# Performance work log

Measured on AMD Instinct MI355X. Metric: run time of the kernel, lower is better.

## Reference

```python
import jax, jax.numpy as jnp
import numpy as np


def lrelu(x):
    return jnp.where(x > 0, x, 0.1 * x)


def setup_inputs() -> dict:
    key = jax.random.key(0)
    ks = jax.random.split(key, 16)
    L, B, E = 160, 16, 512
    C, H, DM, DO = 256, 512, 128, 512  # conv channels, enc_hid, d_mlp, dec_hid

    def rn(k, shape, scale=0.05):
        return jax.random.normal(k, shape, dtype=jnp.float32) * scale

    return {
        "x": rn(ks[0], (L, B, E), 1.0),
        "h": rn(ks[1], (B, H), 1.0),
        "conv_w": rn(ks[2], (C, E, 3)),
        "conv_b": rn(ks[3], (C,)),
        "bn_g": jnp.ones((C,), jnp.float32),
        "bn_b": jnp.zeros((C,), jnp.float32),
        "W1": rn(ks[4], (DM, 2 * (C + 2) + H)),
        "b1": rn(ks[5], (DM,)),
        "W2": rn(ks[6], (DM, DM)), "b2": rn(ks[7], (DM,)),
        "W3": rn(ks[8], (DM, DM)), "b3": rn(ks[9], (DM,)),
        "W4": rn(ks[10], (DM, DM)), "b4": rn(ks[11], (DM,)),
        "W5": rn(ks[12], (DM, DM)), "b5": rn(ks[13], (DM,)),
        "W6": rn(ks[14], (DO, DM)), "b6": rn(ks[15], (DO,)),
    }


def reference(x, h, conv_w, conv_b, bn_g, bn_b,
              W1, b1, W2, b2, W3, b3, W4, b4, W5, b5, W6, b6):
    L, B, E = x.shape
    # --- ConvLayer: Conv1d(k=3, pad=1) -> LeakyReLU(0.1) -> BatchNorm1d (training stats)
    xc = jnp.transpose(x, (1, 2, 0))  # (B, E, L)
    y = jax.lax.conv_general_dilated(xc, conv_w, (1,), [(1, 1)],
                                     dimension_numbers=("NCH", "OIH", "NCH"))
    y = lrelu(y + conv_b[None, :, None])
    mu = y.mean(axis=(0, 2), keepdims=True)
    var = y.var(axis=(0, 2), keepdims=True)  # biased variance (torch training BN)
    y = (y - mu) * jax.lax.rsqrt(var + 1e-5)
    y = y * bn_g[None, :, None] + bn_b[None, :, None]
    y = jnp.transpose(y, (0, 2, 1))  # (B, L, C)

    # --- coordinate features: [(i/sqrt(L)-2)/2, (i % sqrt(L) - 2)/2]
    sL = np.sqrt(L)
    i = jnp.arange(L, dtype=jnp.float32)
    coords = jnp.stack([(i / sL - 2.0) / 2.0, (jnp.mod(i, sL) - 2.0) / 2.0], axis=-1)  # (L, 2)
    xf = jnp.concatenate([y, jnp.broadcast_to(coords[None], (B, L, 2))], axis=-1)  # (B, L, C+2)
    Cp = xf.shape[-1]

    # --- g_mlp first Linear decomposed over [x_i | x_j | h] feature blocks:
    # x_i[b,a,c] = xf[b,c] (varies with dim2); x_j[b,a,c] = cat(xf[b,a], h[b]) (varies with dim1)
    W1i = W1[:, :Cp]            # acts on x_i
    W1jx = W1[:, Cp:2 * Cp]     # acts on x part of x_j
    W1jh = W1[:, 2 * Cp:]       # acts on h part of x_j
    u = jnp.einsum('blc,dc->bld', xf, W1i)                     # (B, L, DM), index = dim2
    v = jnp.einsum('blc,dc->bld', xf, W1jx) + (h @ W1jh.T)[:, None, :]  # (B, L, DM), index = dim1
    z = lrelu(v[:, :, None, :] + u[:, None, :, :] + b1)        # (B, L, L, DM)
    z = lrelu(z @ W2.T + b2)
    z = lrelu(z @ W3.T + b3)
    z = lrelu(z @ W4.T + b4)
    s = z.sum(axis=(1, 2))  # sum over all L*L pairs -> (B, DM)

    # --- f_mlp
    s = lrelu(s @ W5.T + b5)
    return lrelu(s @ W6.T + b6)  # (B, dec_hid)
```

## Files before the change

### kernel.cpp

```cpp
#include <hip/hip_runtime.h>
#include <cstdint>

typedef unsigned short u16;
typedef uint32_t u32;

typedef __bf16 bf16x8 __attribute__((ext_vector_type(8)));
typedef float  f32x2  __attribute__((ext_vector_type(2)));
typedef float  f32x4  __attribute__((ext_vector_type(4)));
typedef float  f32x16 __attribute__((ext_vector_type(16)));
typedef u16    u16x4  __attribute__((ext_vector_type(4)));
typedef u16    u16x8  __attribute__((ext_vector_type(8)));

__device__ __forceinline__ u16 f2bf(float f) {
    u32 x = __float_as_uint(f);
    return (u16)((x + 0x7FFFu + ((x >> 16) & 1u)) >> 16);
}
__device__ __forceinline__ float lrelu(float x) { return fmaxf(x, 0.1f * x); }

__device__ __forceinline__ u32 pack_rn(float lo, float hi) {
    u32 a = __float_as_uint(lo) + 0x8000u;
    u32 b = __float_as_uint(hi) + 0x8000u;
    return __builtin_amdgcn_perm(b, a, 0x07060302u);
}

__global__ __launch_bounds__(256) void k_prep(
    const float* __restrict__ x, const float* __restrict__ conv_w,
    const float* __restrict__ W2, const float* __restrict__ W3, const float* __restrict__ W4,
    const float* __restrict__ b2, const float* __restrict__ b3, const float* __restrict__ b4,
    const float* __restrict__ h, const float* __restrict__ W1,
    u16* __restrict__ xb, u16* __restrict__ wcb_f, u16* __restrict__ wfrag,
    float* __restrict__ W1T4, float* __restrict__ hW)
{
    int blk = blockIdx.x, tid = threadIdx.x;
    if (blk < 1280) {
        int o = (blk * 256 + tid) * 4;
        int e = o & 511;
        int bl = o >> 9;
        int b = bl / 160, l = bl % 160;
        f32x4 v = *(const f32x4*)(x + ((size_t)(l * 16 + b)) * 512 + e);
        u16x4 ov;
        ov[0] = f2bf(v[0]); ov[1] = f2bf(v[1]); ov[2] = f2bf(v[2]); ov[3] = f2bf(v[3]);
        *(u16x4*)&xb[o] = ov;
    } else if (blk < 1472) {
        int g = (blk - 1280) * 256 + tid;
        int lane = g & 63;
        int ks = (g >> 6) % 48;
        int cb = g / 3072;
        int c = cb * 16 + (lane & 15);
        int quad = lane >> 4;
        int k0 = ks * 32 + quad * 8;
        int tap = k0 >> 9, e0 = k0 & 511;
        u16x8 ov;
        #pragma unroll
        for (int j = 0; j < 8; j++)
            ov[j] = f2bf(conv_w[((size_t)c * 512 + e0 + j) * 3 + tap]);
        *(u16x8*)&wcb_f[(size_t)g * 8] = ov;
    } else if (blk < 1526) {
        int o = ((blk - 1472) * 256 + tid) * 4;
        int layer = o / 18432, rem = o % 18432;
        int ks9 = rem >> 11;
        int rem2 = rem & 2047;
        int hh = rem2 >> 10;
        int rem3 = rem2 & 1023;
        int n = rem3 >> 3, j0 = rem3 & 7;
        const float* W = (layer == 0) ? W2 : (layer == 1) ? W3 : W4;
        const float* bi = (layer == 0) ? b2 : (layer == 1) ? b3 : b4;
        u16x4 ov;
        if (ks9 < 8) {
            f32x4 v = *(const f32x4*)(W + (size_t)n * 128 + 16 * ks9 + 8 * hh + j0);
            ov[0] = f2bf(v[0]); ov[1] = f2bf(v[1]); ov[2] = f2bf(v[2]); ov[3] = f2bf(v[3]);
        } else {
            ov[0] = (hh == 0 && j0 == 0) ? f2bf(bi[n]) : (u16)0;
            ov[1] = 0; ov[2] = 0; ov[3] = 0;
        }
        *(u16x4*)&wfrag[o] = ov;
    } else if (blk < 1591) {
        int cq = blk - 1526;
        int t = tid;
        const float* src = (t < 128)
            ? (W1 + (size_t)t * 1028 + cq * 4)
            : (W1 + (size_t)(t - 128) * 1028 + 258 + cq * 4);
        f32x2 v0 = *(const f32x2*)src;
        f32x2 v1 = *(const f32x2*)(src + 2);
        f32x4 v;
        v[0] = v0[0]; v[1] = v0[1];
        v[2] = (cq == 64) ? 0.f : v1[0];
        v[3] = (cq == 64) ? 0.f : v1[1];
        *(f32x4*)&W1T4[((size_t)cq * 256 + t) * 4] = v;
    } else {
        int gid = (blk - 1591) * 256 + tid;
        int outp = gid >> 4, q = gid & 15;
        int b = outp >> 7, d = outp & 127;
        const float* hr = h + (size_t)b * 512;
        const float* wr = W1 + (size_t)d * 1028 + 516;
        float acc = 0.f;
        #pragma unroll
        for (int c = 0; c < 8; c++) {
            int k = c * 64 + q * 4;
            f32x4 hv = *(const f32x4*)(hr + k);
            f32x4 wv = *(const f32x4*)(wr + k);
            acc += hv[0]*wv[0] + hv[1]*wv[1] + hv[2]*wv[2] + hv[3]*wv[3];
        }
        acc += __shfl_xor(acc, 1); acc += __shfl_xor(acc, 2);
        acc += __shfl_xor(acc, 4); acc += __shfl_xor(acc, 8);
        if (q == 0) hW[outp] = acc;
    }
}

__global__ __launch_bounds__(256, 2) void k_conv(
    const u16* __restrict__ xb, const u16* __restrict__ wcb_f,
    const float* __restrict__ conv_b,
    float* __restrict__ ws_y, float* __restrict__ stats)
{
    __shared__ u16 xs[34 * 520];
    int tid = threadIdx.x, wg = blockIdx.x;
    int rowtile = wg >> 2, cg = wg & 3;
    int b = rowtile / 5, l0 = (rowtile % 5) * 32;

    for (int t = tid; t < 34 * 64; t += 256) {
        int s = t >> 6, ch = t & 63;
        int lg = l0 + s - 1;
        u16x8 v = {};
        if (lg >= 0 && lg < 160)
            v = *(const u16x8*)(xb + ((size_t)(b * 160 + lg)) * 512 + ch * 8);
        *(u16x8*)&xs[s * 520 + ch * 8] = v;
    }
    __syncthreads();

    int lane = tid & 63, w = tid >> 6;
    int row16 = lane & 15, quad = lane >> 4;
    int cb = cg * 4 + w;
    int c_n = cb * 16 + row16;
    const u16* wb = wcb_f + (size_t)cb * 24576;

    f32x4 acc0 = {0,0,0,0}, acc1 = {0,0,0,0};
    for (int ks4 = 0; ks4 < 48; ks4 += 4) {
        bf16x8 wf[4];
        #pragma unroll
        for (int q = 0; q < 4; q++)
            wf[q] = *(const bf16x8*)(wb + (size_t)((ks4 + q) * 64 + lane) * 8);
        #pragma unroll
        for (int q = 0; q < 4; q++) {
            int k = (ks4 + q) * 32 + quad * 8;
            int tap = k >> 9, e = k & 511;
            bf16x8 a0 = *(const bf16x8*)&xs[(row16 + tap) * 520 + e];
            bf16x8 a1 = *(const bf16x8*)&xs[(16 + row16 + tap) * 520 + e];
            acc0 = __builtin_amdgcn_mfma_f32_16x16x32_bf16(a0, wf[q], acc0, 0, 0, 0);
            acc1 = __builtin_amdgcn_mfma_f32_16x16x32_bf16(a1, wf[q], acc1, 0, 0, 0);
        }
    }

    float bias = conv_b[c_n];
    float sum = 0.f, sq = 0.f;
    #pragma unroll
    for (int mt = 0; mt < 2; mt++) {
        f32x4 a = mt ? acc1 : acc0;
        #pragma unroll
        for (int r = 0; r < 4; r++) {
            float v = lrelu(a[r] + bias);
            int lr = l0 + mt * 16 + quad * 4 + r;
            ws_y[((size_t)(b * 160 + lr)) * 256 + c_n] = v;
            sum += v; sq += v * v;
        }
    }
    sum += __shfl_xor(sum, 16); sum += __shfl_xor(sum, 32);
    sq  += __shfl_xor(sq, 16);  sq  += __shfl_xor(sq, 32);
    if (quad == 0) {
        atomicAdd(&stats[c_n], sum);
        atomicAdd(&stats[256 + c_n], sq);
    }
}

__global__ __launch_bounds__(256) void k_uv(
    const float* __restrict__ ws_y, const float* __restrict__ stats,
    const float* __restrict__ bn_g, const float* __restrict__ bn_b,
    const float* __restrict__ W1T4, const float* __restrict__ b1,
    const float* __restrict__ hW,
    float* __restrict__ uu, float* __restrict__ vv)
{
    __shared__ float a_s[256], c_s[256];
    __shared__ float xfs[8 * 260];
    int tid = threadIdx.x;
    int row0 = blockIdx.x * 8;
    int b = row0 / 160, l0 = row0 % 160;
    {
        int c = tid;
        float mu  = stats[c] * (1.0f / 2560.0f);
        float var = stats[256 + c] * (1.0f / 2560.0f) - mu * mu;
        float rs  = rsqrtf(var + 1e-5f) * bn_g[c];
        a_s[c] = rs;
        c_s[c] = bn_b[c] - mu * rs;
    }
    __syncthreads();
    float sLf = sqrtf(160.0f);
    for (int idx = tid; idx < 8 * 260; idx += 256) {
        int r = idx / 260, c = idx - r * 260;
        int l = l0 + r;
        float v = 0.f;
        if (c < 256) {
            v = ws_y[((size_t)(b * 160 + l)) * 256 + c] * a_s[c] + c_s[c];
        } else if (c == 256) {
            v = ((float)l / sLf - 2.0f) * 0.5f;
        } else if (c == 257) {
            float fi = (float)l;
            float m = fi - floorf(fi / sLf) * sLf;
            v = (m - 2.0f) * 0.5f;
        }
        xfs[r * 260 + c] = v;
    }
    __syncthreads();

    float acc[8] = {0,0,0,0,0,0,0,0};
    #pragma unroll 4
    for (int cq = 0; cq < 65; cq++) {
        f32x4 w4 = *(const f32x4*)&W1T4[((size_t)cq * 256 + tid) * 4];
        #pragma unroll
        for (int r = 0; r < 8; r++) {
            f32x4 xv = *(const f32x4*)&xfs[r * 260 + cq * 4];
            acc[r] += w4[0]*xv[0] + w4[1]*xv[1] + w4[2]*xv[2] + w4[3]*xv[3];
        }
    }

    bool isv = tid >= 128;
    int d = tid & 127;
    float vadd = isv ? (hW[b * 128 + d] + b1[d]) : 0.f;
    float* dst = isv ? vv : uu;
    #pragma unroll
    for (int r = 0; r < 8; r++)
        dst[((size_t)(b * 160 + l0 + r)) * 128 + d] = acc[r] + vadd;
}

__global__ __launch_bounds__(512, 4) void k_mlp(
    const float* __restrict__ vv, const float* __restrict__ uu,
    const u16* __restrict__ wfrag,
    float* __restrict__ s_glob)
{
    __shared__ __align__(16) u16 Wlds[18432];
    __shared__ float spart[128];
    int tid = threadIdx.x;
    int wave = tid >> 6, lane = tid & 63;
    int h = lane >> 5, lo = lane & 31;
    int b = blockIdx.x / 100, sub = blockIdx.x % 100;
    int tileb = sub * 8 + wave;

    if (tid < 128) spart[tid] = 0.f;

    u32 selv = h ? 0x07060302u : 0x05040100u;
    uint4 biasfrag;
    biasfrag.x = (h == 0) ? 0x00003F80u : 0u;
    biasfrag.y = 0u; biasfrag.z = 0u; biasfrag.w = 0u;

    f32x16 Z;
    #pragma unroll
    for (int r = 0; r < 16; r++) Z[r] = 0.f;

    uint4 B[8], Bn[8];
    float ssum[4];

    int i  = (tileb / 10) * 2  + (lo >> 4);
    int jj = (tileb % 10) * 16 + (lo & 15);
    const float* vr = vv + ((size_t)(b * 160 + i))  * 128 + 8 * h;
    const float* ur = uu + ((size_t)(b * 160 + jj)) * 128 + 8 * h;

    for (int layer = 0; layer < 3; layer++) {
        __syncthreads();
        {
            const uint4* src = (const uint4*)(wfrag + layer * 18432);
            #pragma unroll
            for (int it = 0; it < 5; it++) {
                int idx = it * 512 + tid;
                if (idx < 2304)
                    *(uint4*)&Wlds[idx * 8] = src[idx];
            }
        }
        __syncthreads();

        if (layer == 0) {
            #pragma unroll
            for (int ks = 0; ks < 8; ks++) {
                f32x4 v0 = *(const f32x4*)(vr + 16 * ks);
                f32x4 v1 = *(const f32x4*)(vr + 16 * ks + 4);
                f32x4 u0 = *(const f32x4*)(ur + 16 * ks);
                f32x4 u1 = *(const f32x4*)(ur + 16 * ks + 4);
                uint4 d;
                d.x = pack_rn(lrelu(v0[0]+u0[0]), lrelu(v0[1]+u0[1]));
                d.y = pack_rn(lrelu(v0[2]+u0[2]), lrelu(v0[3]+u0[3]));
                d.z = pack_rn(lrelu(v1[0]+u1[0]), lrelu(v1[1]+u1[1]));
                d.w = pack_rn(lrelu(v1[2]+u1[2]), lrelu(v1[3]+u1[3]));
                B[ks] = d;
            }
        }

        #pragma unroll
        for (int nt = 0; nt < 4; nt++) {
            f32x16 a;
            #pragma unroll
            for (int ks = 0; ks < 9; ks++) {
                bf16x8 wf = *(const bf16x8*)&Wlds[(size_t)(ks * 256 + h * 128 + nt * 32 + lo) * 8];
                uint4 zu = (ks < 8) ? B[ks] : biasfrag;
                bf16x8 zf = *(bf16x8*)&zu;
                if (layer < 2)
                    a = __builtin_amdgcn_mfma_f32_32x32x16_bf16(wf, zf, ks ? a : Z, 0, 0, 0);
                else
                    a = __builtin_amdgcn_mfma_f32_32x32x16_bf16(zf, wf, ks ? a : Z, 0, 0, 0);
            }

            if (layer < 2) {
                u32 own[4][2], oth[4][2];
                #pragma unroll
                for (int c = 0; c < 4; c++)
                    #pragma unroll
                    for (int p = 0; p < 2; p++)
                        own[c][p] = pack_rn(lrelu(a[c + 8*p]),
                                            lrelu(a[c + 4 + 8*p]));
                #pragma unroll
                for (int c = 0; c < 4; c++)
                    #pragma unroll
                    for (int p = 0; p < 2; p++)
                        oth[c][p] = (u32)__shfl_xor((int)own[c][p], 32);
                #pragma unroll
                for (int p = 0; p < 2; p++) {
                    u32 dA0 = __builtin_amdgcn_perm(own[1][p], own[0][p], selv);
                    u32 dB0 = __builtin_amdgcn_perm(oth[1][p], oth[0][p], selv);
                    u32 dA1 = __builtin_amdgcn_perm(own[3][p], own[2][p], selv);
                    u32 dB1 = __builtin_amdgcn_perm(oth[3][p], oth[2][p], selv);
                    uint4 d;
                    d.x = h ? dB0 : dA0;
                    d.y = h ? dB1 : dA1;
                    d.z = h ? dA0 : dB0;
                    d.w = h ? dA1 : dB1;
                    Bn[2 * nt + p] = d;
                }
            } else {
                float t = 0.f;
                #pragma unroll
                for (int r = 0; r < 16; r++)
                    t += lrelu(a[r]);
                ssum[nt] = t;
            }
        }

        if (layer < 2) {
            #pragma unroll
            for (int ks = 0; ks < 8; ks++) B[ks] = Bn[ks];
        }
    }

    #pragma unroll
    for (int nt = 0; nt < 4; nt++) {
        float v = ssum[nt] + __shfl_xor(ssum[nt], 32);
        if (h == 0) atomicAdd(&spart[nt * 32 + lo], v);
    }
    __syncthreads();
    if (tid < 128) atomicAdd(&s_glob[b * 128 + tid], spart[tid]);
}

__global__ __launch_bounds__(256) void k_final(
    const float* __restrict__ s_glob,
    const float* __restrict__ W5, const float* __restrict__ b5,
    const float* __restrict__ W6, const float* __restrict__ b6,
    float* __restrict__ out)
{
    __shared__ float sh[128], t5[128];
    int b = blockIdx.x, tid = threadIdx.x;
    if (tid < 128) sh[tid] = s_glob[b * 128 + tid];
    __syncthreads();
    if (tid < 128) {
        const float* wr = W5 + (size_t)tid * 128;
        float acc = b5[tid];
        #pragma unroll
        for (int k = 0; k < 128; k += 4) {
            f32x4 wv = *(const f32x4*)(wr + k);
            f32x4 sv = *(const f32x4*)&sh[k];
            acc += wv[0]*sv[0] + wv[1]*sv[1] + wv[2]*sv[2] + wv[3]*sv[3];
        }
        t5[tid] = lrelu(acc);
    }
    __syncthreads();
    #pragma unroll
    for (int q = 0; q < 2; q++) {
        int o = q * 256 + tid;
        const float* wr = W6 + (size_t)o * 128;
        float acc = b6[o];
        #pragma unroll
        for (int k = 0; k < 128; k += 4) {
            f32x4 wv = *(const f32x4*)(wr + k);
            f32x4 tv = *(const f32x4*)&t5[k];
            acc += wv[0]*tv[0] + wv[1]*tv[1] + wv[2]*tv[2] + wv[3]*tv[3];
        }
        out[b * 512 + o] = lrelu(acc);
    }
}

extern "C" void kernel_launch(void* const* d_in, const int* in_sizes, int n_in,
                              void* d_out, int out_size, void* d_ws, size_t ws_size,
                              hipStream_t stream)
{
    const float* x      = (const float*)d_in[0];
    const float* h      = (const float*)d_in[1];
    const float* conv_w = (const float*)d_in[2];
    const float* conv_b = (const float*)d_in[3];
    const float* bn_g   = (const float*)d_in[4];
    const float* bn_b   = (const float*)d_in[5];
    const float* W1     = (const float*)d_in[6];
    const float* b1     = (const float*)d_in[7];
    const float* W2     = (const float*)d_in[8];
    const float* b2     = (const float*)d_in[9];
    const float* W3     = (const float*)d_in[10];
    const float* b3     = (const float*)d_in[11];
    const float* W4     = (const float*)d_in[12];
    const float* b4     = (const float*)d_in[13];
    const float* W5     = (const float*)d_in[14];
    const float* b5     = (const float*)d_in[15];
    const float* W6     = (const float*)d_in[16];
    const float* b6     = (const float*)d_in[17];

    char* ws = (char*)d_ws;
    float* s_glob = (float*)(ws + 0);
    float* stats  = (float*)(ws + 8192);
    float* hW     = (float*)(ws + 10240);
    float* ws_y   = (float*)(ws + 18432);
    float* vv     = (float*)(ws + 2639872);
    float* uu     = (float*)(ws + 3950592);
    u16*   xb     = (u16*)  (ws + 5261312);
    u16*   wcb_f  = (u16*)  (ws + 7882752);
    u16*   wfrag  = (u16*)  (ws + 8669184);
    float* W1T4   = (float*)(ws + 8779776);

    hipMemsetAsync(ws, 0, 10240, stream);
    k_prep <<<1719, 256, 0, stream>>>(x, conv_w, W2, W3, W4, b2, b3, b4, h, W1,
                                      xb, wcb_f, wfrag, W1T4, hW);
    k_conv <<<320, 256, 0, stream>>>(xb, wcb_f, conv_b, ws_y, stats);
    k_uv   <<<320, 256, 0, stream>>>(ws_y, stats, bn_g, bn_b, W1T4, b1, hW, uu, vv);
    k_mlp  <<<1600, 512, 0, stream>>>(vv, uu, wfrag, s_glob);
    k_final<<<16, 256, 0, stream>>>(s_glob, W5, b5, W6, b6, (float*)d_out);
}
```

Baseline: 215.5 us.

## Shrink per-block work across conv, uv and MLP kernels; fold memset into prep

Conv blocks now cover 16 rows instead of 32, uv blocks 4 rows instead of 8, and MLP blocks use 4 waves instead of 8, doubling grid sizes for more parallelism and occupancy. The MLP inner loop is reordered so each B fragment feeds four accumulators across nt, which removes the Bn double buffer. The hipMemsetAsync is replaced by extra zeroing blocks in k_prep to save a launch. In exchange, each MLP block's weight load to LDS is amortized over fewer waves, and there is more redundant halo loading in conv.

```diff
diff --git a/kernel.cpp b/kernel.cpp
--- a/kernel.cpp
+++ b/kernel.cpp
@@ -29,7 +29,7 @@
     const float* __restrict__ b2, const float* __restrict__ b3, const float* __restrict__ b4,
     const float* __restrict__ h, const float* __restrict__ W1,
     u16* __restrict__ xb, u16* __restrict__ wcb_f, u16* __restrict__ wfrag,
-    float* __restrict__ W1T4, float* __restrict__ hW)
+    float* __restrict__ W1T4, float* __restrict__ hW, float* __restrict__ zero0)
 {
     int blk = blockIdx.x, tid = threadIdx.x;
     if (blk < 1280) {
@@ -87,7 +87,7 @@
         v[2] = (cq == 64) ? 0.f : v1[0];
         v[3] = (cq == 64) ? 0.f : v1[1];
         *(f32x4*)&W1T4[((size_t)cq * 256 + t) * 4] = v;
-    } else {
+    } else if (blk < 1719) {
         int gid = (blk - 1591) * 256 + tid;
         int outp = gid >> 4, q = gid & 15;
         int b = outp >> 7, d = outp & 127;
@@ -104,20 +104,26 @@
         acc += __shfl_xor(acc, 1); acc += __shfl_xor(acc, 2);
         acc += __shfl_xor(acc, 4); acc += __shfl_xor(acc, 8);
         if (q == 0) hW[outp] = acc;
-    }
-}
-
-__global__ __launch_bounds__(256, 2) void k_conv(
+    } else {
+        int idx = (blk - 1719) * 256 + tid;
+        if (idx < 640) {
+            f32x4 z = {0.f, 0.f, 0.f, 0.f};
+            *(f32x4*)&zero0[idx * 4] = z;
+        }
+    }
+}
+
+__global__ __launch_bounds__(256, 4) void k_conv(
     const u16* __restrict__ xb, const u16* __restrict__ wcb_f,
     const float* __restrict__ conv_b,
     float* __restrict__ ws_y, float* __restrict__ stats)
 {
-    __shared__ u16 xs[34 * 520];
+    __shared__ u16 xs[18 * 520];
     int tid = threadIdx.x, wg = blockIdx.x;
     int rowtile = wg >> 2, cg = wg & 3;
-    int b = rowtile / 5, l0 = (rowtile % 5) * 32;
-
-    for (int t = tid; t < 34 * 64; t += 256) {
+    int b = rowtile / 10, l0 = (rowtile % 10) * 16;
+
+    for (int t = tid; t < 18 * 64; t += 256) {
         int s = t >> 6, ch = t & 63;
         int lg = l0 + s - 1;
         u16x8 v = {};
@@ -133,7 +139,7 @@
     int c_n = cb * 16 + row16;
     const u16* wb = wcb_f + (size_t)cb * 24576;
 
-    f32x4 acc0 = {0,0,0,0}, acc1 = {0,0,0,0};
+    f32x4 acc0 = {0,0,0,0};
     for (int ks4 = 0; ks4 < 48; ks4 += 4) {
         bf16x8 wf[4];
         #pragma unroll
@@ -144,24 +150,18 @@
             int k = (ks4 + q) * 32 + quad * 8;
             int tap = k >> 9, e = k & 511;
             bf16x8 a0 = *(const bf16x8*)&xs[(row16 + tap) * 520 + e];
-            bf16x8 a1 = *(const bf16x8*)&xs[(16 + row16 + tap) * 520 + e];
             acc0 = __builtin_amdgcn_mfma_f32_16x16x32_bf16(a0, wf[q], acc0, 0, 0, 0);
-            acc1 = __builtin_amdgcn_mfma_f32_16x16x32_bf16(a1, wf[q], acc1, 0, 0, 0);
         }
     }
 
     float bias = conv_b[c_n];
     float sum = 0.f, sq = 0.f;
     #pragma unroll
-    for (int mt = 0; mt < 2; mt++) {
-        f32x4 a = mt ? acc1 : acc0;
-        #pragma unroll
-        for (int r = 0; r < 4; r++) {
-            float v = lrelu(a[r] + bias);
-            int lr = l0 + mt * 16 + quad * 4 + r;
-            ws_y[((size_t)(b * 160 + lr)) * 256 + c_n] = v;
-            sum += v; sq += v * v;
-        }
+    for (int r = 0; r < 4; r++) {
+        float v = lrelu(acc0[r] + bias);
+        int lr = l0 + quad * 4 + r;
+        ws_y[((size_t)(b * 160 + lr)) * 256 + c_n] = v;
+        sum += v; sq += v * v;
     }
     sum += __shfl_xor(sum, 16); sum += __shfl_xor(sum, 32);
     sq  += __shfl_xor(sq, 16);  sq  += __shfl_xor(sq, 32);
@@ -179,9 +179,9 @@
     float* __restrict__ uu, float* __restrict__ vv)
 {
     __shared__ float a_s[256], c_s[256];
-    __shared__ float xfs[8 * 260];
+    __shared__ float xfs[4 * 260];
     int tid = threadIdx.x;
-    int row0 = blockIdx.x * 8;
+    int row0 = blockIdx.x * 4;
     int b = row0 / 160, l0 = row0 % 160;
     {
         int c = tid;
@@ -193,7 +193,7 @@
     }
     __syncthreads();
     float sLf = sqrtf(160.0f);
-    for (int idx = tid; idx < 8 * 260; idx += 256) {
+    for (int idx = tid; idx < 4 * 260; idx += 256) {
         int r = idx / 260, c = idx - r * 260;
         int l = l0 + r;
         float v = 0.f;
@@ -210,12 +210,12 @@
     }
     __syncthreads();
 
-    float acc[8] = {0,0,0,0,0,0,0,0};
+    float acc[4] = {0,0,0,0};
     #pragma unroll 4
     for (int cq = 0; cq < 65; cq++) {
         f32x4 w4 = *(const f32x4*)&W1T4[((size_t)cq * 256 + tid) * 4];
         #pragma unroll
-        for (int r = 0; r < 8; r++) {
+        for (int r = 0; r < 4; r++) {
             f32x4 xv = *(const f32x4*)&xfs[r * 260 + cq * 4];
             acc[r] += w4[0]*xv[0] + w4[1]*xv[1] + w4[2]*xv[2] + w4[3]*xv[3];
         }
@@ -226,11 +226,11 @@
     float vadd = isv ? (hW[b * 128 + d] + b1[d]) : 0.f;
     float* dst = isv ? vv : uu;
     #pragma unroll
-    for (int r = 0; r < 8; r++)
+    for (int r = 0; r < 4; r++)
         dst[((size_t)(b * 160 + l0 + r)) * 128 + d] = acc[r] + vadd;
 }
 
-__global__ __launch_bounds__(512, 4) void k_mlp(
+__global__ __launch_bounds__(256, 4) void k_mlp(
     const float* __restrict__ vv, const float* __restrict__ uu,
     const u16* __restrict__ wfrag,
     float* __restrict__ s_glob)
@@ -240,8 +240,8 @@
     int tid = threadIdx.x;
     int wave = tid >> 6, lane = tid & 63;
     int h = lane >> 5, lo = lane & 31;
-    int b = blockIdx.x / 100, sub = blockIdx.x % 100;
-    int tileb = sub * 8 + wave;
+    int b = blockIdx.x / 200, sub = blockIdx.x % 200;
+    int tileb = sub * 4 + wave;
 
     if (tid < 128) spart[tid] = 0.f;
 
@@ -250,11 +250,8 @@
     biasfrag.x = (h == 0) ? 0x00003F80u : 0u;
     biasfrag.y = 0u; biasfrag.z = 0u; biasfrag.w = 0u;
 
-    f32x16 Z;
-    #pragma unroll
-    for (int r = 0; r < 16; r++) Z[r] = 0.f;
-
-    uint4 B[8], Bn[8];
+    uint4 B[8];
+    f32x16 acc[4];
     float ssum[4];
 
     int i  = (tileb / 10) * 2  + (lo >> 4);
@@ -267,10 +264,9 @@
         {
             const uint4* src = (const uint4*)(wfrag + layer * 18432);
             #pragma unroll
-            for (int it = 0; it < 5; it++) {
-                int idx = it * 512 + tid;
-                if (idx < 2304)
-                    *(uint4*)&Wlds[idx * 8] = src[idx];
+            for (int it = 0; it < 9; it++) {
+                int idx = it * 256 + tid;
+                *(uint4*)&Wlds[idx * 8] = src[idx];
             }
         }
         __syncthreads();
@@ -292,27 +288,34 @@
         }
 
         #pragma unroll
-        for (int nt = 0; nt < 4; nt++) {
-            f32x16 a;
-            #pragma unroll
-            for (int ks = 0; ks < 9; ks++) {
+        for (int nt = 0; nt < 4; nt++)
+            #pragma unroll
+            for (int r = 0; r < 16; r++) acc[nt][r] = 0.f;
+
+        #pragma unroll
+        for (int ks = 0; ks < 9; ks++) {
+            uint4 zu = (ks < 8) ? B[ks] : biasfrag;
+            bf16x8 zf = *(bf16x8*)&zu;
+            #pragma unroll
+            for (int nt = 0; nt < 4; nt++) {
                 bf16x8 wf = *(const bf16x8*)&Wlds[(size_t)(ks * 256 + h * 128 + nt * 32 + lo) * 8];
-                uint4 zu = (ks < 8) ? B[ks] : biasfrag;
-                bf16x8 zf = *(bf16x8*)&zu;
                 if (layer < 2)
-                    a = __builtin_amdgcn_mfma_f32_32x32x16_bf16(wf, zf, ks ? a : Z, 0, 0, 0);
+                    acc[nt] = __builtin_amdgcn_mfma_f32_32x32x16_bf16(wf, zf, acc[nt], 0, 0, 0);
                 else
-                    a = __builtin_amdgcn_mfma_f32_32x32x16_bf16(zf, wf, ks ? a : Z, 0, 0, 0);
+                    acc[nt] = __builtin_amdgcn_mfma_f32_32x32x16_bf16(zf, wf, acc[nt], 0, 0, 0);
             }
-
-            if (layer < 2) {
+        }
+
+        if (layer < 2) {
+            #pragma unroll
+            for (int nt = 0; nt < 4; nt++) {
                 u32 own[4][2], oth[4][2];
                 #pragma unroll
                 for (int c = 0; c < 4; c++)
                     #pragma unroll
                     for (int p = 0; p < 2; p++)
-                        own[c][p] = pack_rn(lrelu(a[c + 8*p]),
-                                            lrelu(a[c + 4 + 8*p]));
+                        own[c][p] = pack_rn(lrelu(acc[nt][c + 8*p]),
+                                            lrelu(acc[nt][c + 4 + 8*p]));
                 #pragma unroll
                 for (int c = 0; c < 4; c++)
                     #pragma unroll
@@ -329,20 +332,18 @@
                     d.y = h ? dB1 : dA1;
                     d.z = h ? dA0 : dB0;
                     d.w = h ? dA1 : dB1;
-                    Bn[2 * nt + p] = d;
+                    B[2 * nt + p] = d;
                 }
-            } else {
+            }
+        } else {
+            #pragma unroll
+            for (int nt = 0; nt < 4; nt++) {
                 float t = 0.f;
                 #pragma unroll
                 for (int r = 0; r < 16; r++)
-                    t += lrelu(a[r]);
+                    t += lrelu(acc[nt][r]);
                 ssum[nt] = t;
             }
-        }
-
-        if (layer < 2) {
-            #pragma unroll
-            for (int ks = 0; ks < 8; ks++) B[ks] = Bn[ks];
         }
     }
 
@@ -427,11 +428,10 @@
     u16*   wfrag  = (u16*)  (ws + 8669184);
     float* W1T4   = (float*)(ws + 8779776);
 
-    hipMemsetAsync(ws, 0, 10240, stream);
-    k_prep <<<1719, 256, 0, stream>>>(x, conv_w, W2, W3, W4, b2, b3, b4, h, W1,
-                                      xb, wcb_f, wfrag, W1T4, hW);
-    k_conv <<<320, 256, 0, stream>>>(xb, wcb_f, conv_b, ws_y, stats);
-    k_uv   <<<320, 256, 0, stream>>>(ws_y, stats, bn_g, bn_b, W1T4, b1, hW, uu, vv);
-    k_mlp  <<<1600, 512, 0, stream>>>(vv, uu, wfrag, s_glob);
+    k_prep <<<1722, 256, 0, stream>>>(x, conv_w, W2, W3, W4, b2, b3, b4, h, W1,
+                                      xb, wcb_f, wfrag, W1T4, hW, s_glob);
+    k_conv <<<640, 256, 0, stream>>>(xb, wcb_f, conv_b, ws_y, stats);
+    k_uv   <<<640, 256, 0, stream>>>(ws_y, stats, bn_g, bn_b, W1T4, b1, hW, uu, vv);
+    k_mlp  <<<3200, 256, 0, stream>>>(vv, uu, wfrag, s_glob);
     k_final<<<16, 256, 0, stream>>>(s_glob, W5, b5, W6, b6, (float*)d_out);
 }
```

After: 217.3 us. No clear change (+0.8%).
